# Optimization experiments

Measured on AMD Instinct MI355X. Metric: run time of the kernel, lower is better.

Reference implementation:

```python
import jax, jax.numpy as jnp
import numpy as np

N_NODES = 100000
NNZ = 3200000


def setup_inputs() -> dict:
    key = jax.random.key(0)
    k1, k2, k3, k4 = jax.random.split(key, 4)
    x = jax.random.normal(k1, (N_NODES, 256), dtype=jnp.float32)
    lap_rows = jax.random.randint(k2, (NNZ,), 0, N_NODES, dtype=jnp.int32)
    lap_cols = jax.random.randint(k3, (NNZ,), 0, N_NODES, dtype=jnp.int32)
    lap_vals = jax.random.normal(k4, (NNZ,), dtype=jnp.float32)
    return {"x": x, "lap_rows": lap_rows, "lap_cols": lap_cols, "lap_vals": lap_vals}


def reference(x, lap_rows, lap_cols, lap_vals):
    # Lx via COO SpMM: gather rows of x by col index, scale, scatter-add by row index.
    # messages: [nnz, F]
    msgs = lap_vals[:, None] * x[lap_cols]
    lx = jax.ops.segment_sum(msgs, lap_rows, num_segments=x.shape[0])  # [N, F]
    # trace(X^T L X) == sum(X \u2299 LX); identical math to dense mm + trace, no N x F x F matmul.
    nnz = lap_vals.shape[0]
    bias = jnp.sum(x * lx) / nnz
    return bias
```

## Files before the change

kernel.cpp:

```cpp
#include <hip/hip_runtime.h>

#define THREADS 256
#define WPB (THREADS / 64)
#define RPB 64
#define CGRP 8
#define MAXKEY 12504
#define CAPS 320
#define CHUNK 6250
#define EPT 25
#define OVF_CAP 8192

typedef _Float16 h2 __attribute__((ext_vector_type(2)));
union H2U { unsigned u; h2 h; _Float16 s[2]; };

#if defined(__has_builtin)
#if __has_builtin(__builtin_amdgcn_fdot2)
#define HAVE_FDOT2 1
#endif
#endif
#ifdef HAVE_FDOT2
__device__ __forceinline__ float fdot2(unsigned a, unsigned b, float c) {
    H2U ua, ub; ua.u = a; ub.u = b;
    return __builtin_amdgcn_fdot2(ua.h, ub.h, c, false);
}
#else
__device__ __forceinline__ float fdot2(unsigned a, unsigned b, float c) {
    H2U ua, ub; ua.u = a; ub.u = b;
    return fmaf((float)ua.s[1], (float)ub.s[1], fmaf((float)ua.s[0], (float)ub.s[0], c));
}
#endif

__global__ void init_acc_kernel(double* acc) { *acc = 0.0; }

__global__ __launch_bounds__(THREADS) void quant_kernel(
    const float* __restrict__ x, unsigned short* __restrict__ xh, int n4)
{
    int i = blockIdx.x * blockDim.x + threadIdx.x;
    const int st = gridDim.x * blockDim.x;
    for (; i < n4; i += st) {
        float4 v = ((const float4*)x)[i];
        H2U p0, p1;
        p0.s[0] = (_Float16)v.x; p0.s[1] = (_Float16)v.y;
        p1.s[0] = (_Float16)v.z; p1.s[1] = (_Float16)v.w;
        uint2 o; o.x = p0.u; o.y = p1.u;
        ((uint2*)xh)[i] = o;
    }
}

__device__ __forceinline__ int edge_key(int r, int c, int cdiv) {
    int cg = c / cdiv;
    if (cg > CGRP - 1) cg = CGRP - 1;
    return (r >> 6) * CGRP + cg;
}

__global__ __launch_bounds__(THREADS) void bin_kernel(
    const int* __restrict__ rows, const int* __restrict__ cols,
    const float* __restrict__ vals, unsigned* __restrict__ cur,
    uint2* __restrict__ rec, unsigned* __restrict__ ovf_cnt,
    uint4* __restrict__ ovf, int nnz, int nkey, int cdiv)
{
    __shared__ unsigned hcnt[MAXKEY];
    const int tid = threadIdx.x;
    for (int k = tid; k < nkey; k += THREADS) hcnt[k] = 0u;
    __syncthreads();

    const int cbase = blockIdx.x * CHUNK;
    const int cend  = min(cbase + CHUNK, nnz);
    unsigned short rnk[EPT];

    #pragma unroll
    for (int i = 0; i < EPT; ++i) {
        int e = cbase + tid + i * THREADS;
        rnk[i] = 0;
        if (e < cend) {
            int key = edge_key(rows[e], cols[e], cdiv);
            rnk[i] = (unsigned short)atomicAdd(&hcnt[key], 1u);
        }
    }
    __syncthreads();

    for (int k = tid; k < nkey; k += THREADS) {
        unsigned c = hcnt[k];
        unsigned gs = 0;
        if (c) gs = atomicAdd(&cur[k], c);
        hcnt[k] = gs;
    }
    __syncthreads();

    #pragma unroll
    for (int i = 0; i < EPT; ++i) {
        int e = cbase + tid + i * THREADS;
        if (e < cend) {
            int r = rows[e], c = cols[e];
            int key = edge_key(r, c, cdiv);
            unsigned pos = hcnt[key] + (unsigned)rnk[i];
            if (pos < CAPS) {
                uint2 m;
                m.x = (unsigned)c | ((unsigned)(r & (RPB - 1)) << 17);
                m.y = __float_as_uint(vals[e]);
                rec[(size_t)key * CAPS + pos] = m;
            } else {
                unsigned oi = atomicAdd(ovf_cnt, 1u);
                if (oi < OVF_CAP) {
                    uint4 m4; m4.x = (unsigned)r; m4.y = (unsigned)c;
                    m4.z = __float_as_uint(vals[e]); m4.w = 0u;
                    ovf[oi] = m4;
                }
            }
        }
    }
}

__global__ __launch_bounds__(THREADS) void edge_lds_kernel(
    const unsigned short* __restrict__ xh, const uint2* __restrict__ rec,
    const unsigned* __restrict__ cur, double* __restrict__ acc, int nodes)
{
    __shared__ unsigned short lrow[RPB * 256];
    __shared__ unsigned s_pre[CGRP + 1];
    __shared__ float wsum[WPB];
    const int b     = blockIdx.x;
    const int rbase = b * RPB;
    const int nrow  = min(RPB, nodes - rbase);
    const int tid   = threadIdx.x;

    if (tid < CGRP) {
        unsigned c = cur[b * CGRP + tid];
        s_pre[tid + 1] = (c > CAPS) ? (unsigned)CAPS : c;
    }
    const int4* src = (const int4*)(xh + (size_t)rbase * 256);
    int4* dst = (int4*)lrow;
    const int nv = nrow * 32;
    for (int t = tid; t < nv; t += THREADS) dst[t] = src[t];
    __syncthreads();
    if (tid == 0) {
        unsigned a = 0;
        s_pre[0] = 0;
        #pragma unroll
        for (int k = 1; k <= CGRP; ++k) { a += s_pre[k]; s_pre[k] = a; }
    }
    __syncthreads();

    const int lane = tid & 63;
    const int wid  = tid >> 6;
    const int half = lane >> 5;
    const int hl   = lane & 31;
    const unsigned T = s_pre[CGRP];
    const unsigned nbatch = (T + 63) >> 6;
    const unsigned base_rec = (unsigned)b * CGRP * CAPS;

    float lacc0 = 0.0f, lacc1 = 0.0f;

    for (unsigned t = wid; t < nbatch; t += WPB) {
        unsigned f = (t << 6) + (unsigned)lane;
        unsigned lo = 0; float v = 0.0f;
        if (f < T) {
            int cg = 0;
            #pragma unroll
            for (int k = 1; k < CGRP; ++k) cg += (f >= s_pre[k]);
            unsigned idx = f - s_pre[cg];
            uint2 m = rec[base_rec + (unsigned)cg * CAPS + idx];
            lo = m.x; v = __uint_as_float(m.y);
        }
        #pragma unroll 8
        for (int j = 0; j < 32; ++j) {
            const int ei = (j << 1) + half;
            unsigned loj = __shfl(lo, ei);
            float    vj  = __shfl(v, ei);
            const int cj  = (int)(loj & 0x1FFFFu);
            const int rlj = (int)(loj >> 17);
            uint4 ra = ((const uint4*)(lrow + rlj * 256))[hl];
            uint4 cb = ((const uint4*)(xh + (size_t)cj * 256))[hl];
            float s = fdot2(ra.x, cb.x, 0.0f);
            s = fdot2(ra.y, cb.y, s);
            s = fdot2(ra.z, cb.z, s);
            s = fdot2(ra.w, cb.w, s);
            if (j & 1) lacc1 = fmaf(vj, s, lacc1);
            else       lacc0 = fmaf(vj, s, lacc0);
        }
    }

    float lacc = lacc0 + lacc1;
    #pragma unroll
    for (int o = 32; o > 0; o >>= 1) lacc += __shfl_down(lacc, o);
    if (lane == 0) wsum[wid] = lacc;
    __syncthreads();
    if (tid == 0) {
        float bs = 0.0f;
        #pragma unroll
        for (int w = 0; w < WPB; ++w) bs += wsum[w];
        atomicAdd(acc, (double)bs);
    }
}

__global__ __launch_bounds__(THREADS) void ovf_kernel(
    const unsigned short* __restrict__ xh, const unsigned* __restrict__ ovf_cnt,
    const uint4* __restrict__ ovf, double* __restrict__ acc)
{
    __shared__ float wsum[WPB];
    const int lane = threadIdx.x & 63;
    const int wid  = threadIdx.x >> 6;
    const unsigned n = min(*ovf_cnt, (unsigned)OVF_CAP);
    float lacc = 0.0f;
    for (unsigned i = wid; i < n; i += WPB) {
        uint4 m = ovf[i];
        const unsigned r = m.x, c = m.y;
        const float v = __uint_as_float(m.z);
        uint2 a4 = ((const uint2*)(xh + (size_t)r * 256))[lane];
        uint2 b4 = ((const uint2*)(xh + (size_t)c * 256))[lane];
        float s = fdot2(a4.x, b4.x, 0.0f);
        s = fdot2(a4.y, b4.y, s);
        lacc = fmaf(v, s, lacc);
    }
    #pragma unroll
    for (int o = 32; o > 0; o >>= 1) lacc += __shfl_down(lacc, o);
    if (lane == 0) wsum[wid] = lacc;
    __syncthreads();
    if (threadIdx.x == 0) {
        float bs = 0.0f;
        #pragma unroll
        for (int w = 0; w < WPB; ++w) bs += wsum[w];
        if (n) atomicAdd(acc, (double)bs);
    }
}

__global__ __launch_bounds__(THREADS) void edge_dot_q_kernel(
    const unsigned short* __restrict__ xh,
    const int* __restrict__ rows, const int* __restrict__ cols,
    const float* __restrict__ vals, double* __restrict__ acc, int nnz)
{
    __shared__ float wsum[WPB];
    const int lane  = threadIdx.x & 63;
    const int wid   = threadIdx.x >> 6;
    const int gwave = blockIdx.x * WPB + wid;
    const int nwave = gridDim.x * WPB;
    float lacc = 0.0f;
    for (int base = gwave * 64; base < nnz; base += nwave * 64) {
        int e = base + lane;
        int r = 0, c = 0; float v = 0.0f;
        if (e < nnz) { r = rows[e]; c = cols[e]; v = vals[e]; }
        #pragma unroll 8
        for (int j = 0; j < 64; ++j) {
            int rj = __shfl(r, j); int cj = __shfl(c, j); float vj = __shfl(v, j);
            uint2 a4 = ((const uint2*)(xh + (size_t)rj * 256))[lane];
            uint2 b4 = ((const uint2*)(xh + (size_t)cj * 256))[lane];
            float s = fdot2(a4.x, b4.x, 0.0f);
            s = fdot2(a4.y, b4.y, s);
            lacc = fmaf(vj, s, lacc);
        }
    }
    #pragma unroll
    for (int o = 32; o > 0; o >>= 1) lacc += __shfl_down(lacc, o);
    if (lane == 0) wsum[wid] = lacc;
    __syncthreads();
    if (threadIdx.x == 0) {
        float bs = 0.0f;
        #pragma unroll
        for (int w = 0; w < WPB; ++w) bs += wsum[w];
        atomicAdd(acc, (double)bs);
    }
}

__global__ __launch_bounds__(THREADS) void edge_dot_kernel(
    const float* __restrict__ x,
    const int* __restrict__ rows, const int* __restrict__ cols,
    const float* __restrict__ vals, double* __restrict__ acc, int nnz)
{
    __shared__ float wsum[WPB];
    const int lane  = threadIdx.x & 63;
    const int wid   = threadIdx.x >> 6;
    const int gwave = blockIdx.x * WPB + wid;
    const int nwave = gridDim.x * WPB;
    float lacc = 0.0f;
    for (int base = gwave * 64; base < nnz; base += nwave * 64) {
        int e = base + lane;
        int r = 0, c = 0; float v = 0.0f;
        if (e < nnz) { r = rows[e]; c = cols[e]; v = vals[e]; }
        #pragma unroll 4
        for (int j = 0; j < 64; ++j) {
            int rj = __shfl(r, j); int cj = __shfl(c, j); float vj = __shfl(v, j);
            const float4 a = ((const float4*)(x + (size_t)rj * 256))[lane];
            const float4 b = ((const float4*)(x + (size_t)cj * 256))[lane];
            float s = a.x * b.x;
            s = fmaf(a.y, b.y, s);
            s = fmaf(a.z, b.z, s);
            s = fmaf(a.w, b.w, s);
            lacc = fmaf(vj, s, lacc);
        }
    }
    #pragma unroll
    for (int o = 32; o > 0; o >>= 1) lacc += __shfl_down(lacc, o);
    if (lane == 0) wsum[wid] = lacc;
    __syncthreads();
    if (threadIdx.x == 0) {
        float bs = 0.0f;
        #pragma unroll
        for (int w = 0; w < WPB; ++w) bs += wsum[w];
        atomicAdd(acc, (double)bs);
    }
}

__global__ void finalize_kernel(const double* __restrict__ acc,
                                float* __restrict__ out, int nnz)
{
    out[0] = (float)(*acc / (double)nnz);
}

static inline size_t align256(size_t x) { return (x + 255) & ~(size_t)255; }

extern "C" void kernel_launch(void* const* d_in, const int* in_sizes, int n_in,
                              void* d_out, int out_size, void* d_ws, size_t ws_size,
                              hipStream_t stream) {
    const float* x    = (const float*)d_in[0];
    const int*   rows = (const int*)d_in[1];
    const int*   cols = (const int*)d_in[2];
    const float* vals = (const float*)d_in[3];
    const int nnz   = in_sizes[1];
    const int nelem = in_sizes[0];
    const int nodes = nelem / 256;

    const int nbuck = (nodes + RPB - 1) / RPB;
    const int nkey  = nbuck * CGRP;
    const int cdiv  = (nodes + CGRP - 1) / CGRP;

    double* acc = (double*)d_ws;
    float*  out = (float*)d_out;

    size_t o_xh   = 256;
    size_t o_rec  = align256(o_xh  + (size_t)nelem * 2);
    size_t o_cur  = align256(o_rec + (size_t)nkey * CAPS * 8);
    size_t o_ovfc = align256(o_cur + (size_t)nkey * 4);
    size_t o_ovf  = align256(o_ovfc + 4);
    size_t need_bin   = o_ovf + (size_t)OVF_CAP * 16;
    size_t need_quant = o_xh + (size_t)nelem * 2;

    init_acc_kernel<<<1, 1, 0, stream>>>(acc);

    if (ws_size >= need_bin && nkey <= MAXKEY) {
        unsigned short* xh  = (unsigned short*)((char*)d_ws + o_xh);
        uint2*          rec = (uint2*)((char*)d_ws + o_rec);
        unsigned*       cur = (unsigned*)((char*)d_ws + o_cur);
        unsigned*       ovc = (unsigned*)((char*)d_ws + o_ovfc);
        uint4*          ovf = (uint4*)((char*)d_ws + o_ovf);

        hipMemsetAsync(cur, 0, (size_t)nkey * 4, stream);
        hipMemsetAsync(ovc, 0, 4, stream);
        quant_kernel<<<2048, THREADS, 0, stream>>>(x, xh, nelem / 4);
        const int nbb = (nnz + CHUNK - 1) / CHUNK;
        bin_kernel<<<nbb, THREADS, 0, stream>>>(rows, cols, vals, cur, rec, ovc, ovf, nnz, nkey, cdiv);
        edge_lds_kernel<<<nbuck, THREADS, 0, stream>>>(xh, rec, cur, acc, nodes);
        ovf_kernel<<<1, THREADS, 0, stream>>>(xh, ovc, ovf, acc);
    } else if (ws_size >= need_quant) {
        unsigned short* xh = (unsigned short*)((char*)d_ws + o_xh);
        quant_kernel<<<2048, THREADS, 0, stream>>>(x, xh, nelem / 4);
        edge_dot_q_kernel<<<2048, THREADS, 0, stream>>>(xh, rows, cols, vals, acc, nnz);
    } else {
        edge_dot_kernel<<<2048, THREADS, 0, stream>>>(x, rows, cols, vals, acc, nnz);
    }

    finalize_kernel<<<1, 1, 0, stream>>>(acc, out, nnz);
}
```

Measured before the change: 316.1 us.

## Gather row tiles from global memory with batched loads, cache edges in binning

The edge kernel no longer stages the 64-row fp16 tile into LDS. It reads row vectors straight from global memory and issues eight row/column loads ahead of the dot products to raise memory-level parallelism. The binning kernel keeps rows/cols/vals in registers between its two passes instead of re-reading them, and uses half-size chunks to run more blocks. The zero-init kernel is replaced with a memset. Dropping the LDS tile frees shared memory for occupancy but adds global/L2 traffic for the row operands, and the deeper register arrays may raise register pressure.

```diff
diff --git a/kernel.cpp b/kernel.cpp
--- a/kernel.cpp
+++ b/kernel.cpp
@@ -6,9 +6,10 @@
 #define CGRP 8
 #define MAXKEY 12504
 #define CAPS 320
-#define CHUNK 6250
-#define EPT 25
+#define CHUNK 3125
+#define EPT 13
 #define OVF_CAP 8192
+#define DEPTH 8
 
 typedef _Float16 h2 __attribute__((ext_vector_type(2)));
 union H2U { unsigned u; h2 h; _Float16 s[2]; };
@@ -30,8 +31,6 @@
 }
 #endif
 
-__global__ void init_acc_kernel(double* acc) { *acc = 0.0; }
-
 __global__ __launch_bounds__(THREADS) void quant_kernel(
     const float* __restrict__ x, unsigned short* __restrict__ xh, int n4)
 {
@@ -47,12 +46,6 @@
     }
 }
 
-__device__ __forceinline__ int edge_key(int r, int c, int cdiv) {
-    int cg = c / cdiv;
-    if (cg > CGRP - 1) cg = CGRP - 1;
-    return (r >> 6) * CGRP + cg;
-}
-
 __global__ __launch_bounds__(THREADS) void bin_kernel(
     const int* __restrict__ rows, const int* __restrict__ cols,
     const float* __restrict__ vals, unsigned* __restrict__ cur,
@@ -66,15 +59,22 @@
 
     const int cbase = blockIdx.x * CHUNK;
     const int cend  = min(cbase + CHUNK, nnz);
-    unsigned short rnk[EPT];
+    unsigned mx[EPT], kr[EPT];
+    float    vv[EPT];
 
     #pragma unroll
     for (int i = 0; i < EPT; ++i) {
         int e = cbase + tid + i * THREADS;
-        rnk[i] = 0;
+        kr[i] = 0xFFFFFFFFu;
         if (e < cend) {
-            int key = edge_key(rows[e], cols[e], cdiv);
-            rnk[i] = (unsigned short)atomicAdd(&hcnt[key], 1u);
+            int r = rows[e], c = cols[e];
+            float v = vals[e];
+            int cg = c / cdiv; if (cg > CGRP - 1) cg = CGRP - 1;
+            int key = (r >> 6) * CGRP + cg;
+            unsigned rk = atomicAdd(&hcnt[key], 1u);
+            mx[i] = (unsigned)c | ((unsigned)(r & (RPB - 1)) << 17);
+            kr[i] = ((unsigned)key << 16) | rk;
+            vv[i] = v;
         }
     }
     __syncthreads();
@@ -89,21 +89,19 @@
 
     #pragma unroll
     for (int i = 0; i < EPT; ++i) {
-        int e = cbase + tid + i * THREADS;
-        if (e < cend) {
-            int r = rows[e], c = cols[e];
-            int key = edge_key(r, c, cdiv);
-            unsigned pos = hcnt[key] + (unsigned)rnk[i];
+        if (kr[i] != 0xFFFFFFFFu) {
+            unsigned key = kr[i] >> 16;
+            unsigned pos = hcnt[key] + (kr[i] & 0xFFFFu);
             if (pos < CAPS) {
-                uint2 m;
-                m.x = (unsigned)c | ((unsigned)(r & (RPB - 1)) << 17);
-                m.y = __float_as_uint(vals[e]);
+                uint2 m; m.x = mx[i]; m.y = __float_as_uint(vv[i]);
                 rec[(size_t)key * CAPS + pos] = m;
             } else {
                 unsigned oi = atomicAdd(ovf_cnt, 1u);
                 if (oi < OVF_CAP) {
-                    uint4 m4; m4.x = (unsigned)r; m4.y = (unsigned)c;
-                    m4.z = __float_as_uint(vals[e]); m4.w = 0u;
+                    uint4 m4;
+                    m4.x = ((key >> 3) << 6) | (mx[i] >> 17);
+                    m4.y = mx[i] & 0x1FFFFu;
+                    m4.z = __float_as_uint(vv[i]); m4.w = 0u;
                     ovf[oi] = m4;
                 }
             }
@@ -111,30 +109,22 @@
     }
 }
 
-__global__ __launch_bounds__(THREADS) void edge_lds_kernel(
+__global__ __launch_bounds__(THREADS) void edge_gather_kernel(
     const unsigned short* __restrict__ xh, const uint2* __restrict__ rec,
-    const unsigned* __restrict__ cur, double* __restrict__ acc, int nodes)
-{
-    __shared__ unsigned short lrow[RPB * 256];
+    const unsigned* __restrict__ cur, double* __restrict__ acc)
+{
     __shared__ unsigned s_pre[CGRP + 1];
     __shared__ float wsum[WPB];
-    const int b     = blockIdx.x;
-    const int rbase = b * RPB;
-    const int nrow  = min(RPB, nodes - rbase);
-    const int tid   = threadIdx.x;
+    const int b   = blockIdx.x;
+    const int tid = threadIdx.x;
 
     if (tid < CGRP) {
         unsigned c = cur[b * CGRP + tid];
         s_pre[tid + 1] = (c > CAPS) ? (unsigned)CAPS : c;
     }
-    const int4* src = (const int4*)(xh + (size_t)rbase * 256);
-    int4* dst = (int4*)lrow;
-    const int nv = nrow * 32;
-    for (int t = tid; t < nv; t += THREADS) dst[t] = src[t];
     __syncthreads();
     if (tid == 0) {
-        unsigned a = 0;
-        s_pre[0] = 0;
+        unsigned a = 0; s_pre[0] = 0;
         #pragma unroll
         for (int k = 1; k <= CGRP; ++k) { a += s_pre[k]; s_pre[k] = a; }
     }
@@ -147,6 +137,7 @@
     const unsigned T = s_pre[CGRP];
     const unsigned nbatch = (T + 63) >> 6;
     const unsigned base_rec = (unsigned)b * CGRP * CAPS;
+    const size_t rowbase = (size_t)b * RPB * 256;
 
     float lacc0 = 0.0f, lacc1 = 0.0f;
 
@@ -161,21 +152,28 @@
             uint2 m = rec[base_rec + (unsigned)cg * CAPS + idx];
             lo = m.x; v = __uint_as_float(m.y);
         }
-        #pragma unroll 8
-        for (int j = 0; j < 32; ++j) {
-            const int ei = (j << 1) + half;
-            unsigned loj = __shfl(lo, ei);
-            float    vj  = __shfl(v, ei);
-            const int cj  = (int)(loj & 0x1FFFFu);
-            const int rlj = (int)(loj >> 17);
-            uint4 ra = ((const uint4*)(lrow + rlj * 256))[hl];
-            uint4 cb = ((const uint4*)(xh + (size_t)cj * 256))[hl];
-            float s = fdot2(ra.x, cb.x, 0.0f);
-            s = fdot2(ra.y, cb.y, s);
-            s = fdot2(ra.z, cb.z, s);
-            s = fdot2(ra.w, cb.w, s);
-            if (j & 1) lacc1 = fmaf(vj, s, lacc1);
-            else       lacc0 = fmaf(vj, s, lacc0);
+        #pragma unroll
+        for (int j0 = 0; j0 < 32; j0 += DEPTH) {
+            uint4 ra[DEPTH], cb[DEPTH];
+            #pragma unroll
+            for (int u = 0; u < DEPTH; ++u) {
+                const int ei = ((j0 + u) << 1) + half;
+                unsigned loj = __shfl(lo, ei);
+                const int cj = (int)(loj & 0x1FFFFu);
+                const int rl = (int)(loj >> 17);
+                ra[u] = ((const uint4*)(xh + rowbase + (size_t)rl * 256))[hl];
+                cb[u] = ((const uint4*)(xh + (size_t)cj * 256))[hl];
+            }
+            #pragma unroll
+            for (int u = 0; u < DEPTH; ++u) {
+                float vj = __shfl(v, ((j0 + u) << 1) + half);
+                float s = fdot2(ra[u].x, cb[u].x, 0.0f);
+                s = fdot2(ra[u].y, cb[u].y, s);
+                s = fdot2(ra[u].z, cb[u].z, s);
+                s = fdot2(ra[u].w, cb[u].w, s);
+                if (u & 1) lacc1 = fmaf(vj, s, lacc1);
+                else       lacc0 = fmaf(vj, s, lacc0);
+            }
         }
     }
 
@@ -333,7 +331,7 @@
     size_t need_bin   = o_ovf + (size_t)OVF_CAP * 16;
     size_t need_quant = o_xh + (size_t)nelem * 2;
 
-    init_acc_kernel<<<1, 1, 0, stream>>>(acc);
+    hipMemsetAsync(acc, 0, 8, stream);
 
     if (ws_size >= need_bin && nkey <= MAXKEY) {
         unsigned short* xh  = (unsigned short*)((char*)d_ws + o_xh);
@@ -347,7 +345,7 @@
         quant_kernel<<<2048, THREADS, 0, stream>>>(x, xh, nelem / 4);
         const int nbb = (nnz + CHUNK - 1) / CHUNK;
         bin_kernel<<<nbb, THREADS, 0, stream>>>(rows, cols, vals, cur, rec, ovc, ovf, nnz, nkey, cdiv);
-        edge_lds_kernel<<<nbuck, THREADS, 0, stream>>>(xh, rec, cur, acc, nodes);
+        edge_gather_kernel<<<nbuck, THREADS, 0, stream>>>(xh, rec, cur, acc);
         ovf_kernel<<<1, THREADS, 0, stream>>>(xh, ovc, ovf, acc);
     } else if (ws_size >= need_quant) {
         unsigned short* xh = (unsigned short*)((char*)d_ws + o_xh);
```

Result: slower. 465.3 us (+47.2%).
